# Kernel tuning notes

Hardware: AMD Instinct MI355X
Metric: run time of the kernel (lower is better)

Reference implementation:

```python
import jax, jax.numpy as jnp
import numpy as np

B, C = 1048576, 32
NEG_WEIGHT = 1.0
EPS = 1e-7


def setup_inputs() -> dict:
    key = jax.random.key(0)
    k1, k2 = jax.random.split(key)
    logits = jax.random.normal(k1, (B, C), dtype=jnp.float32)
    target = jax.random.uniform(k2, (B, C), dtype=jnp.float32)
    return {"logits": logits, "target": target}


def reference(logits, target):
    # pred = clamp(sigmoid(logits), eps, 1-eps)
    pred = jnp.clip(jax.nn.sigmoid(logits), EPS, 1.0 - EPS)
    logp = jnp.log(pred)          # [B, C]
    log1mp = jnp.log(1.0 - pred)  # [B, C]

    labels = jnp.argmax(target, axis=1)  # [B]

    # Branch label == 0: mean over classes of full soft-BCE
    loss0 = jnp.mean(target * logp + (1.0 - target) * log1mp, axis=1)  # [B]

    # Branch label != 0: target[i,label]*log(pred[i,label]) + neg_w*log(1-pred[i,0])
    rows = jnp.arange(target.shape[0])
    t_lab = target[rows, labels]
    logp_lab = logp[rows, labels]
    loss1 = t_lab * logp_lab + NEG_WEIGHT * log1mp[:, 0]  # [B]

    per_row = jnp.where(labels == 0, loss0, loss1)  # [B]
    # reduction == 'mean'
    return -jnp.mean(per_row)
```

## Files before the change

kernel.cpp:

```cpp
#include <hip/hip_runtime.h>
#include <math.h>

#define C_EPS 1e-7f

__global__ void zero_out_kernel(float* out) { out[0] = 0.0f; }

__global__ __launch_bounds__(256) void softbce_kernel(
    const float* __restrict__ logits,
    const float* __restrict__ target,
    float* __restrict__ out,
    int B)
{
    const int tid    = blockIdx.x * blockDim.x + threadIdx.x;
    const int lane   = threadIdx.x & 63;
    const int wave   = tid >> 6;
    const int nWaves = (gridDim.x * blockDim.x) >> 6;
    const int nChunks = B >> 3;
    const int sub     = lane & 7;
    const int colBase = sub * 4;

    float acc = 0.0f;

    for (int c = wave; c < nChunks; c += nWaves) {
        const float4 tg = ((const float4*)target)[(size_t)c * 64 + lane];
        const float4 lg = ((const float4*)logits)[(size_t)c * 64 + lane];

        float tv[4] = {tg.x, tg.y, tg.z, tg.w};
        float xv[4] = {lg.x, lg.y, lg.z, lg.w};

        float rs   = 0.0f;
        float bv   = -INFINITY;
        int   bi   = 0;
        float bp   = 0.0f;
        float l1p0 = 0.0f;

        #pragma unroll
        for (int j = 0; j < 4; ++j) {
            float x = xv[j];
            float t = tv[j];
            float p = 1.0f / (1.0f + __expf(-x));
            p = fminf(fmaxf(p, C_EPS), 1.0f - C_EPS);
            float lp  = __logf(p);
            float l1p = __logf(1.0f - p);
            rs += t * lp + (1.0f - t) * l1p;
            if (j == 0) l1p0 = l1p;
            if (t > bv) { bv = t; bi = colBase + j; bp = t * lp; }
        }

        rs += __shfl_xor(rs, 1);
        rs += __shfl_xor(rs, 2);
        rs += __shfl_xor(rs, 4);

        #pragma unroll
        for (int d = 1; d <= 4; d <<= 1) {
            float ov = __shfl_xor(bv, d);
            int   oi = __shfl_xor(bi, d);
            float op = __shfl_xor(bp, d);
            if (ov > bv || (ov == bv && oi < bi)) { bv = ov; bi = oi; bp = op; }
        }

        float z0 = __shfl(l1p0, lane & 56);

        float loss = (bi == 0) ? rs * (1.0f / 32.0f) : (bp + z0);

        if (sub == 0) acc += loss;
    }

    #pragma unroll
    for (int d = 1; d < 64; d <<= 1) acc += __shfl_xor(acc, d);

    __shared__ float sacc[4];
    if (lane == 0) sacc[threadIdx.x >> 6] = acc;
    __syncthreads();
    if (threadIdx.x == 0) {
        float s = sacc[0] + sacc[1] + sacc[2] + sacc[3];
        float scale = -1.0f / (float)B;
        atomicAdd(out, s * scale);
    }
}

extern "C" void kernel_launch(void* const* d_in, const int* in_sizes, int n_in,
                              void* d_out, int out_size, void* d_ws, size_t ws_size,
                              hipStream_t stream) {
    const float* logits = (const float*)d_in[0];
    const float* target = (const float*)d_in[1];
    float* out = (float*)d_out;

    const int B = in_sizes[0] / 32;

    zero_out_kernel<<<1, 1, 0, stream>>>(out);

    const int blocks = 4096;
    softbce_kernel<<<blocks, 256, 0, stream>>>(logits, target, out, B);
}
```

Baseline: 284.5 us.

## Process one row per thread and compute log-sigmoid in log domain

Each thread now handles a whole 32-column row, so the cross-lane shuffles for the row sum and argmax are gone, and the launch grows to one thread per row with 4096 blocks of work each. The two logs and the reciprocal are replaced by a single exp2 and log2 softplus form, with clamping done in log space. In exchange, each thread's loads stride 128 bytes across lanes instead of being contiguous, which can hurt coalescing. The new log-domain clamping and the plain greater-than argmax tie-break may differ slightly from the reference.

```diff
diff --git a/kernel.cpp b/kernel.cpp
--- a/kernel.cpp
+++ b/kernel.cpp
@@ -1,9 +1,24 @@
 #include <hip/hip_runtime.h>
 #include <math.h>
 
-#define C_EPS 1e-7f
+
+#define LOG_EPS   -16.118095651f
+#define LOG_1MEPS -1.1920929e-07f
 
 __global__ void zero_out_kernel(float* out) { out[0] = 0.0f; }
+
+__device__ __forceinline__ void elem(float x, float t, int col,
+                                     float& rs, float& bv, int& bi,
+                                     float& lpmax, float& l1p0)
+{
+    float e   = __builtin_exp2f(x * -1.44269504f);
+    float lpu = __builtin_log2f(1.0f + e) * -0.69314718f;
+    float lp  = fminf(fmaxf(lpu,     LOG_EPS), LOG_1MEPS);
+    float l1p = fminf(fmaxf(lpu - x, LOG_EPS), LOG_1MEPS);
+    rs = fmaf(t, lp - l1p, rs + l1p);
+    if (col == 0) l1p0 = l1p;
+    if (t > bv) { bv = t; bi = col; lpmax = lp; }
+}
 
 __global__ __launch_bounds__(256) void softbce_kernel(
     const float* __restrict__ logits,
@@ -11,71 +26,42 @@
     float* __restrict__ out,
     int B)
 {
-    const int tid    = blockIdx.x * blockDim.x + threadIdx.x;
-    const int lane   = threadIdx.x & 63;
-    const int wave   = tid >> 6;
-    const int nWaves = (gridDim.x * blockDim.x) >> 6;
-    const int nChunks = B >> 3;
-    const int sub     = lane & 7;
-    const int colBase = sub * 4;
+    const int row = blockIdx.x * 256 + threadIdx.x;
 
     float acc = 0.0f;
+    if (row < B) {
+        const float4* tg = (const float4*)target + (size_t)row * 8;
+        const float4* lg = (const float4*)logits + (size_t)row * 8;
 
-    for (int c = wave; c < nChunks; c += nWaves) {
-        const float4 tg = ((const float4*)target)[(size_t)c * 64 + lane];
-        const float4 lg = ((const float4*)logits)[(size_t)c * 64 + lane];
+        float4 T[8], X[8];
+        #pragma unroll
+        for (int j = 0; j < 8; ++j) T[j] = tg[j];
+        #pragma unroll
+        for (int j = 0; j < 8; ++j) X[j] = lg[j];
 
-        float tv[4] = {tg.x, tg.y, tg.z, tg.w};
-        float xv[4] = {lg.x, lg.y, lg.z, lg.w};
-
-        float rs   = 0.0f;
-        float bv   = -INFINITY;
-        int   bi   = 0;
-        float bp   = 0.0f;
-        float l1p0 = 0.0f;
-
+        float rs = 0.0f, bv = -INFINITY, lpmax = 0.0f, l1p0 = 0.0f;
+        int   bi = 0;
         #pragma unroll
-        for (int j = 0; j < 4; ++j) {
-            float x = xv[j];
-            float t = tv[j];
-            float p = 1.0f / (1.0f + __expf(-x));
-            p = fminf(fmaxf(p, C_EPS), 1.0f - C_EPS);
-            float lp  = __logf(p);
-            float l1p = __logf(1.0f - p);
-            rs += t * lp + (1.0f - t) * l1p;
-            if (j == 0) l1p0 = l1p;
-            if (t > bv) { bv = t; bi = colBase + j; bp = t * lp; }
+        for (int j = 0; j < 8; ++j) {
+            elem(X[j].x, T[j].x, 4*j + 0, rs, bv, bi, lpmax, l1p0);
+            elem(X[j].y, T[j].y, 4*j + 1, rs, bv, bi, lpmax, l1p0);
+            elem(X[j].z, T[j].z, 4*j + 2, rs, bv, bi, lpmax, l1p0);
+            elem(X[j].w, T[j].w, 4*j + 3, rs, bv, bi, lpmax, l1p0);
         }
 
-        rs += __shfl_xor(rs, 1);
-        rs += __shfl_xor(rs, 2);
-        rs += __shfl_xor(rs, 4);
-
-        #pragma unroll
-        for (int d = 1; d <= 4; d <<= 1) {
-            float ov = __shfl_xor(bv, d);
-            int   oi = __shfl_xor(bi, d);
-            float op = __shfl_xor(bp, d);
-            if (ov > bv || (ov == bv && oi < bi)) { bv = ov; bi = oi; bp = op; }
-        }
-
-        float z0 = __shfl(l1p0, lane & 56);
-
-        float loss = (bi == 0) ? rs * (1.0f / 32.0f) : (bp + z0);
-
-        if (sub == 0) acc += loss;
+        acc = (bi == 0) ? rs * (1.0f / 32.0f) : fmaf(bv, lpmax, l1p0);
     }
 
     #pragma unroll
     for (int d = 1; d < 64; d <<= 1) acc += __shfl_xor(acc, d);
 
     __shared__ float sacc[4];
+    const int lane = threadIdx.x & 63;
     if (lane == 0) sacc[threadIdx.x >> 6] = acc;
     __syncthreads();
     if (threadIdx.x == 0) {
         float s = sacc[0] + sacc[1] + sacc[2] + sacc[3];
-        float scale = -1.0f / (float)B;
-        atomicAdd(out, s * scale);
+        atomicAdd(out, s * (-1.0f / (float)B));
     }
 }
 
@@ -89,7 +75,5 @@
     const int B = in_sizes[0] / 32;
 
     zero_out_kernel<<<1, 1, 0, stream>>>(out);
-
-    const int blocks = 4096;
-    softbce_kernel<<<blocks, 256, 0, stream>>>(logits, target, out, B);
+    softbce_kernel<<<(B + 255) / 256, 256, 0, stream>>>(logits, target, out, B);
 }
```

Measured after the change: 282.2 us. No clear change (-0.8%).
